# Kernel tuning notes

Hardware: AMD Instinct MI355X
Metric: run time of the kernel (lower is better)

## Reference

```python
import jax, jax.numpy as jnp
import jax.scipy.linalg as jsp
import numpy as np

# Problem dimensions (match init_kwargs P_shape/A_shape)
N = 256   # variables
M = 512   # constraints
B = 64    # batch

# OSQP ADMM hyper-parameters (fixed-rho variant of the OSQP algorithm)
SIGMA = 1e-6
RHO = 0.1
ALPHA = 1.6
N_ITERS = 500


def setup_inputs() -> dict:
    key = jax.random.key(0)
    kP, kq, kA, kc = jax.random.split(key, 4)
    # P is diagonal with strictly positive entries -> PSD (values are the nnz of P)
    P_val = jax.random.uniform(kP, (B, N), dtype=jnp.float32) + 0.1
    q_val = jax.random.normal(kq, (B, N), dtype=jnp.float32)
    # A is a dense pattern; values stored row-major as its nnz vector
    A_val = jax.random.normal(kA, (B, M * N), dtype=jnp.float32) / np.sqrt(N)
    # Feasible box: l <= u by construction
    center = jax.random.normal(kc, (B, M), dtype=jnp.float32)
    l_val = center - 1.0
    u_val = center + 1.0
    return {"P_val": P_val, "q_val": q_val, "A_val": A_val, "l_val": l_val, "u_val": u_val}


def _admm_qp(P_val, q_val, A_val, l_val, u_val):
    """Batched OSQP-style ADMM solve of min 1/2 x'Px + q'x  s.t. l <= Ax <= u.

    P is diagonal (nnz pattern = diag), A is dense (nnz pattern = full m x n).
    """
    A = A_val.reshape(B, M, N)                      # [B,m,n]
    # KKT-like matrix M_k = P + sigma*I + rho*A'A   [B,n,n]
    eye = jnp.eye(N, dtype=P_val.dtype)
    P_diag = P_val + SIGMA                          # diagonal of P + sigma*I
    Mk = RHO * jnp.einsum('bmi,bmj->bij', A, A) + jax.vmap(jnp.diag)(P_diag)
    L = jnp.linalg.cholesky(Mk)                     # [B,n,n], factor once, reuse
    Lt = jnp.swapaxes(L, -1, -2)

    def kkt_solve(rhs):                             # rhs [B,n]
        y1 = jsp.solve_triangular(L, rhs[..., None], lower=True)
        y2 = jsp.solve_triangular(Lt, y1, lower=False)
        return y2[..., 0]

    x0 = jnp.zeros((B, N), dtype=P_val.dtype)
    z0 = jnp.zeros((B, M), dtype=P_val.dtype)
    y0 = jnp.zeros((B, M), dtype=P_val.dtype)

    def step(state, _):
        x, z, y = state
        rhs = SIGMA * x - q_val + jnp.einsum('bmn,bm->bn', A, RHO * z - y)
        x_t = kkt_solve(rhs)                        # x-tilde
        z_t = jnp.einsum('bmn,bn->bm', A, x_t)      # z-tilde = A x_t
        x_new = ALPHA * x_t + (1.0 - ALPHA) * x
        z_hat = ALPHA * z_t + (1.0 - ALPHA) * z
        z_new = jnp.clip(z_hat + y / RHO, l_val, u_val)
        y_new = y + RHO * (z_hat - z_new)
        return (x_new, z_new, y_new), None

    (x, _, _), _ = jax.lax.scan(step, (x0, z0, y0), None, length=N_ITERS)
    return x


def reference(P_val, q_val, A_val, l_val, u_val):
    return _admm_qp(P_val, q_val, A_val, l_val, u_val)   # [B, n] primal solutions
```

## Files before the change

kernel.cpp:

```cpp
#include <hip/hip_runtime.h>
#include <hip/hip_fp16.h>

#define N_VAR 256
#define M_CON 512
#define BATCH 64
#define SIGMA_C 1e-6f
#define RHO_C 0.1f
#define ALPHA_C 1.6f
#define NITERS 500

__global__ __launch_bounds__(256) void k_transpose(const float* __restrict__ A,
                                                   float* __restrict__ At) {
  __shared__ float tile[32][33];
  int b = blockIdx.z;
  int n0 = blockIdx.x * 32;
  int m0 = blockIdx.y * 32;
  const float* Ab = A + (size_t)b * (M_CON * N_VAR);
  float* Atb = At + (size_t)b * (M_CON * N_VAR);
  int tx = threadIdx.x, ty = threadIdx.y;
#pragma unroll
  for (int j = 0; j < 32; j += 8)
    tile[ty + j][tx] = Ab[(size_t)(m0 + ty + j) * N_VAR + n0 + tx];
  __syncthreads();
#pragma unroll
  for (int j = 0; j < 32; j += 8)
    Atb[(size_t)(n0 + ty + j) * M_CON + m0 + tx] = tile[tx][ty + j];
}

__global__ __launch_bounds__(256) void k_ntgemm(
    const float* __restrict__ X, const float* __restrict__ Y,
    float* __restrict__ C, int J, int K,
    long long bsX, long long bsY, long long bsC, float alpha,
    const float* __restrict__ diagv, int tilesJ, int symN) {
  int b = blockIdx.y;
  int ti, tj;
  if (symN > 0) {
    int r = blockIdx.x;
    ti = 0;
    while (r >= symN - ti) { r -= (symN - ti); ++ti; }
    tj = ti + r;
  } else {
    ti = blockIdx.x / tilesJ;
    tj = blockIdx.x % tilesJ;
  }
  int i0 = ti * 128, j0 = tj * 128;
  const float* Xb = X + (size_t)b * bsX;
  const float* Yb = Y + (size_t)b * bsY;
  float* Cb = C + (size_t)b * bsC;
  __shared__ float Xs[2][16][132];
  __shared__ float Ys[2][16][132];
  int tid = threadIdx.x;
  int tx = tid & 15, ty = tid >> 4;
  int row0 = tid >> 2, k40 = (tid & 3) * 4;

  float acc[8][8];
#pragma unroll
  for (int r = 0; r < 8; ++r)
#pragma unroll
    for (int c = 0; c < 8; ++c) acc[r][c] = 0.0f;

  float4 rx0, rx1, ry0, ry1;
  auto prefetch = [&](int kk) {
    rx0 = *(const float4*)(Xb + (size_t)(i0 + row0) * K + kk + k40);
    rx1 = *(const float4*)(Xb + (size_t)(i0 + row0 + 64) * K + kk + k40);
    ry0 = *(const float4*)(Yb + (size_t)(j0 + row0) * K + kk + k40);
    ry1 = *(const float4*)(Yb + (size_t)(j0 + row0 + 64) * K + kk + k40);
  };
  auto commit = [&](int buf) {
    Xs[buf][k40 + 0][row0] = rx0.x; Xs[buf][k40 + 1][row0] = rx0.y;
    Xs[buf][k40 + 2][row0] = rx0.z; Xs[buf][k40 + 3][row0] = rx0.w;
    Xs[buf][k40 + 0][row0 + 64] = rx1.x; Xs[buf][k40 + 1][row0 + 64] = rx1.y;
    Xs[buf][k40 + 2][row0 + 64] = rx1.z; Xs[buf][k40 + 3][row0 + 64] = rx1.w;
    Ys[buf][k40 + 0][row0] = ry0.x; Ys[buf][k40 + 1][row0] = ry0.y;
    Ys[buf][k40 + 2][row0] = ry0.z; Ys[buf][k40 + 3][row0] = ry0.w;
    Ys[buf][k40 + 0][row0 + 64] = ry1.x; Ys[buf][k40 + 1][row0 + 64] = ry1.y;
    Ys[buf][k40 + 2][row0 + 64] = ry1.z; Ys[buf][k40 + 3][row0 + 64] = ry1.w;
  };

  int nkt = K >> 4;
  prefetch(0);
  commit(0);
  __syncthreads();

  for (int kt = 0; kt < nkt; ++kt) {
    int cur = kt & 1;
    if (kt + 1 < nkt) prefetch((kt + 1) * 16);
#pragma unroll
    for (int k = 0; k < 16; ++k) {
      float xr[8], yr[8];
      *(float4*)&xr[0] = *(float4*)&Xs[cur][k][ty * 8];
      *(float4*)&xr[4] = *(float4*)&Xs[cur][k][ty * 8 + 4];
      *(float4*)&yr[0] = *(float4*)&Ys[cur][k][tx * 8];
      *(float4*)&yr[4] = *(float4*)&Ys[cur][k][tx * 8 + 4];
#pragma unroll
      for (int r = 0; r < 8; ++r)
#pragma unroll
        for (int c = 0; c < 8; ++c) acc[r][c] += xr[r] * yr[c];
    }
    if (kt + 1 < nkt) commit(cur ^ 1);
    __syncthreads();
  }

#pragma unroll
  for (int r = 0; r < 8; ++r) {
    int gi = i0 + ty * 8 + r;
#pragma unroll
    for (int c = 0; c < 8; ++c) {
      int gj = j0 + tx * 8 + c;
      float val = acc[r][c] * alpha;
      if (diagv != nullptr && gi == gj) val += diagv[(size_t)b * N_VAR + gi] + SIGMA_C;
      Cb[(size_t)gi * J + gj] = val;
    }
  }
}

__global__ __launch_bounds__(256) void k_mirror(float* __restrict__ C, int n,
                                                long long bsC) {
  __shared__ float tile[32][33];
  int b = blockIdx.y;
  int idx = blockIdx.x;
  int bi = 1;
  while (idx >= bi) { idx -= bi; ++bi; }
  int bj = idx;
  float* Cb = C + (size_t)b * bsC;
  int tx = threadIdx.x & 31, ty = threadIdx.x >> 5;
#pragma unroll
  for (int j = 0; j < 32; j += 8)
    tile[ty + j][tx] = Cb[(size_t)(bj * 32 + ty + j) * n + bi * 32 + tx];
  __syncthreads();
#pragma unroll
  for (int j = 0; j < 32; j += 8)
    Cb[(size_t)(bi * 32 + ty + j) * n + bj * 32 + tx] = tile[tx][ty + j];
}

__global__ __launch_bounds__(512, 2) void k_invert(const float* __restrict__ Mk,
                                                   float* __restrict__ Mi) {
  int b = blockIdx.x;
  const float* src = Mk + (size_t)b * 65536;
  float* dst = Mi + (size_t)b * 65536;
  int t = threadIdx.x;
  int c = t & 255, rh = t >> 8;

  float a[128];
#pragma unroll
  for (int j = 0; j < 128; ++j) a[j] = src[(size_t)(rh * 128 + j) * 256 + c];

  __shared__ float colPan[256][8];
  __shared__ float rowPan[2][8][260];
  __shared__ float PiSh[64];
  __shared__ float Rp[8][260];

  int rh_s = __builtin_amdgcn_readfirstlane(rh);
  int cw_s = __builtin_amdgcn_readfirstlane((t >> 6) & 3);

  if (rh == 0) {
#pragma unroll
    for (int j = 0; j < 8; ++j) rowPan[0][j][c] = a[j];
  }
  __syncthreads();

  for (int s = 0; s < 32; ++s) {
    int kb = s * 8;
    int cur = s & 1, nxt = cur ^ 1;
    int kh = kb >> 7, kj = kb & 127;
    int khn = (kb + 8) >> 7, kjn = (kb + 8) & 127;
    bool mycol = (c >= kb) && (c < kb + 8);

    if (cw_s == (kb >> 6)) {
      if (mycol) {
        int f = c - kb;
#pragma unroll
        for (int j = 0; j < 128; ++j) colPan[rh * 128 + j][f] = a[j];
      }
    }
    if (t < 64) {
      int e = t >> 3, f = t & 7;
      float p = rowPan[cur][e][kb + f];
#pragma unroll
      for (int k2 = 0; k2 < 8; ++k2) {
        float piv = __shfl(p, k2 * 8 + k2);
        float rv = __shfl(p, k2 * 8 + f);
        float cv = __shfl(p, e * 8 + k2);
        float pivinv = 1.0f / piv;
        float srv = rv * pivinv;
        float gen = p - cv * srv;
        p = gen;
        if (e == k2) p = srv;
        if (f == k2) p = -cv * pivinv;
        if (e == k2 && f == k2) p = pivinv;
      }
      PiSh[t] = p;
    }
    __syncthreads();

    float rpan[8];
#pragma unroll
    for (int f2 = 0; f2 < 8; ++f2) rpan[f2] = rowPan[cur][f2][c];
    float rp[8];
#pragma unroll
    for (int e = 0; e < 8; ++e) {
      float4 p0 = *(const float4*)&PiSh[e * 8];
      float4 p1 = *(const float4*)&PiSh[e * 8 + 4];
      rp[e] = p0.x * rpan[0] + p0.y * rpan[1] + p0.z * rpan[2] + p0.w * rpan[3] +
              p1.x * rpan[4] + p1.y * rpan[5] + p1.z * rpan[6] + p1.w * rpan[7];
    }
    if (cw_s == (kb >> 6)) {
      if (mycol) {
        int f = c - kb;
#pragma unroll
        for (int e = 0; e < 8; ++e) rp[e] = PiSh[e * 8 + f];
      }
    }
#pragma unroll
    for (int e = 0; e < 8; ++e) Rp[e][c] = rp[e];

    bool myhalfk = (rh_s == kh);
    bool stashw = (s != 31) && (rh_s == khn);
#pragma unroll
    for (int j = 0; j < 128; ++j) {
      float4 c0 = *(const float4*)&colPan[rh * 128 + j][0];
      float4 c1 = *(const float4*)&colPan[rh * 128 + j][4];
      float aold = a[j];
      float nv = aold -
                 (c0.x * rp[0] + c0.y * rp[1] + c0.z * rp[2] + c0.w * rp[3] +
                  c1.x * rp[4] + c1.y * rp[5] + c1.z * rp[6] + c1.w * rp[7]);
      if (mycol) nv -= aold;
      if (myhalfk && j >= kj && j < kj + 8)
        nv = Rp[j - kj][c];
      a[j] = nv;
      if (stashw && j >= kjn && j < kjn + 8)
        rowPan[nxt][j - kjn][c] = nv;
    }
    __syncthreads();
  }

#pragma unroll
  for (int j = 0; j < 128; ++j) dst[(size_t)(rh * 128 + j) * 256 + c] = a[j];
}

__global__ __launch_bounds__(256) void k_matvec_h(const float* __restrict__ Mi,
                                                  const float* __restrict__ q,
                                                  float* __restrict__ h) {
  int b = blockIdx.x, t = threadIdx.x;
  __shared__ float qs[256];
  qs[t] = q[(size_t)b * 256 + t];
  __syncthreads();
  const float* Mb = Mi + (size_t)b * 65536;
  float acc = 0.0f;
  for (int k = 0; k < 256; ++k) acc += Mb[(size_t)k * 256 + t] * qs[k];
  h[(size_t)b * 256 + t] = acc;
}

__global__ __launch_bounds__(512) void k_matvec_d(const float* __restrict__ At,
                                                  const float* __restrict__ h,
                                                  float* __restrict__ d) {
  int b = blockIdx.x, t = threadIdx.x;
  __shared__ float hs[256];
  if (t < 256) hs[t] = h[(size_t)b * 256 + t];
  __syncthreads();
  const float* Ab = At + (size_t)b * 131072;
  float acc = 0.0f;
  for (int n = 0; n < 256; ++n) acc += Ab[(size_t)n * 512 + t] * hs[n];
  d[(size_t)b * 512 + t] = acc;
}

__global__ __launch_bounds__(512, 2) void k_admm4(
    const float* __restrict__ G, const float* __restrict__ dvec,
    const float* __restrict__ lv, const float* __restrict__ uv,
    unsigned long long* __restrict__ wtag, float* __restrict__ Sbuf) {
  int g = blockIdx.x;
  int b = (g & 7) + 8 * ((g >> 3) & 7);
  int s = g >> 6;
  int t = threadIdx.x;
  int r = t & 31, ck = t >> 5;
  int c0 = ck * 32;

  __shared__ __align__(16) float wloc[512];
  __shared__ float part[16][132];

  const float* Gb = G + (size_t)b * 262144;
  float Greg[4][32];
#pragma unroll
  for (int k = 0; k < 4; ++k) {
    const float* gp = Gb + (size_t)(s * 128 + r + 32 * k) * 512 + c0;
#pragma unroll
    for (int j = 0; j < 8; ++j) {
      float4 v = *(const float4*)(gp + 4 * j);
      Greg[k][4 * j + 0] = v.x; Greg[k][4 * j + 1] = v.y;
      Greg[k][4 * j + 2] = v.z; Greg[k][4 * j + 3] = v.w;
    }
  }

  float zreg = 0.0f, yreg = 0.0f, Sreg = 0.0f;
  float lreg = 0.0f, ureg = 0.0f, dreg = 0.0f;
  if (t < 128) {
    lreg = lv[(size_t)b * 512 + s * 128 + t];
    ureg = uv[(size_t)b * 512 + s * 128 + t];
    dreg = dvec[(size_t)b * 512 + s * 128 + t];
  }
  wloc[t] = 0.0f;

  unsigned long long* wt0 = wtag + (size_t)b * 512;
  unsigned long long* wt1 = wtag + 32768 + (size_t)b * 512;
  int gr = (s * 128 + t) & 511;
  const float4* wq4 = (const float4*)(wloc + c0);

  for (int it = 0; it < NITERS; ++it) {
    __syncthreads();

    float a0 = 0.f, a1 = 0.f, a2 = 0.f, a3 = 0.f;
#pragma unroll
    for (int j = 0; j < 8; ++j) {
      float4 w4 = wq4[j];
      a0 += Greg[0][4 * j + 0] * w4.x + Greg[0][4 * j + 1] * w4.y +
            Greg[0][4 * j + 2] * w4.z + Greg[0][4 * j + 3] * w4.w;
      a1 += Greg[1][4 * j + 0] * w4.x + Greg[1][4 * j + 1] * w4.y +
            Greg[1][4 * j + 2] * w4.z + Greg[1][4 * j + 3] * w4.w;
      a2 += Greg[2][4 * j + 0] * w4.x + Greg[2][4 * j + 1] * w4.y +
            Greg[2][4 * j + 2] * w4.z + Greg[2][4 * j + 3] * w4.w;
      a3 += Greg[3][4 * j + 0] * w4.x + Greg[3][4 * j + 1] * w4.y +
            Greg[3][4 * j + 2] * w4.z + Greg[3][4 * j + 3] * w4.w;
    }
    part[ck][r] = a0;
    part[ck][r + 32] = a1;
    part[ck][r + 64] = a2;
    part[ck][r + 96] = a3;
    __syncthreads();

    if (t < 128) {
      float w_old = RHO_C * zreg - yreg;
      Sreg = w_old - 0.6f * Sreg;
      float p = 0.0f;
#pragma unroll
      for (int c = 0; c < 16; ++c) p += part[c][t];
      float zt = p - dreg;
      float zh = ALPHA_C * zt + (1.0f - ALPHA_C) * zreg;
      float zc = zh + yreg * (1.0f / RHO_C);
      zc = fminf(fmaxf(zc, lreg), ureg);
      yreg += RHO_C * (zh - zc);
      zreg = zc;
      float wn = RHO_C * zreg - yreg;
      wloc[s * 128 + t] = wn;
      if (it < NITERS - 1) {
        unsigned long long pk =
            ((unsigned long long)(unsigned)(it + 1) << 32) |
            (unsigned long long)__float_as_uint(wn);
        unsigned long long* wp = ((it + 1) & 1) ? wt1 : wt0;
        __hip_atomic_store(&wp[s * 128 + t], pk, __ATOMIC_RELAXED,
                           __HIP_MEMORY_SCOPE_AGENT);
      }
    } else if (it < NITERS - 1) {
      unsigned long long* wp = ((it + 1) & 1) ? wt1 : wt0;
      unsigned want = (unsigned)(it + 1);
      unsigned long long v;
      for (;;) {
        v = __hip_atomic_load(&wp[gr], __ATOMIC_RELAXED,
                              __HIP_MEMORY_SCOPE_AGENT);
        if ((unsigned)(v >> 32) == want) break;
        __builtin_amdgcn_s_sleep(1);
      }
      wloc[gr] = __uint_as_float((unsigned)(v & 0xffffffffu));
    }
  }

  if (t < 128) Sbuf[(size_t)b * 512 + s * 128 + t] = Sreg;
}

__global__ __launch_bounds__(256) void k_final(
    const float* __restrict__ A, const float* __restrict__ q,
    const float* __restrict__ Mi, const float* __restrict__ Sbuf,
    float* __restrict__ xout) {
  int b = blockIdx.x, t = threadIdx.x;
  __shared__ float Ssh[512];
  __shared__ float uu[256];
  for (int i = t; i < 512; i += 256) Ssh[i] = Sbuf[(size_t)b * 512 + i];
  __syncthreads();
  const float* Ab = A + (size_t)b * 131072;
  float acc = 0.0f;
  for (int m = 0; m < 512; ++m) acc += Ab[(size_t)m * 256 + t] * Ssh[m];
  uu[t] = ALPHA_C * acc - q[(size_t)b * 256 + t];
  __syncthreads();
  const float* Mb = Mi + (size_t)b * 65536;
  float x = 0.0f;
  for (int kk = 0; kk < 256; ++kk) x += Mb[(size_t)kk * 256 + t] * uu[kk];
  xout[(size_t)b * 256 + t] = x;
}

extern "C" void kernel_launch(void* const* d_in, const int* in_sizes, int n_in,
                              void* d_out, int out_size, void* d_ws, size_t ws_size,
                              hipStream_t stream) {
  (void)in_sizes; (void)n_in; (void)out_size; (void)ws_size;
  const float* P = (const float*)d_in[0];
  const float* q = (const float*)d_in[1];
  const float* Av = (const float*)d_in[2];
  const float* lv = (const float*)d_in[3];
  const float* uv = (const float*)d_in[4];
  float* xout = (float*)d_out;

  float* ws = (float*)d_ws;
  float* At = ws;
  float* F  = ws;
  float* Mi = ws + 8388608;
  float* Mk = ws + 12582912;
  float* G  = ws + 12582912;
  float* hv = ws + 29360128;
  float* dv = ws + 29376512;
  float* Sbuf = ws + 29409280;
  unsigned long long* wtag = (unsigned long long*)ws;

  k_transpose<<<dim3(8, 16, 64), dim3(32, 8), 0, stream>>>(Av, At);
  k_ntgemm<<<dim3(3, 64), 256, 0, stream>>>(At, At, Mk, 256, 512,
                                            131072LL, 131072LL, 65536LL,
                                            RHO_C, P, 0, 2);
  k_mirror<<<dim3(28, 64), 256, 0, stream>>>(Mk, 256, 65536LL);
  k_invert<<<64, 512, 0, stream>>>(Mk, Mi);
  k_matvec_h<<<64, 256, 0, stream>>>(Mi, q, hv);
  k_matvec_d<<<64, 512, 0, stream>>>(At, hv, dv);
  k_ntgemm<<<dim3(8, 64), 256, 0, stream>>>(Av, Mi, F, 256, 256,
                                            131072LL, 65536LL, 131072LL,
                                            1.0f, nullptr, 2, 0);
  k_ntgemm<<<dim3(10, 64), 256, 0, stream>>>(F, Av, G, 512, 256,
                                             131072LL, 131072LL, 262144LL,
                                             1.0f, nullptr, 0, 4);
  k_mirror<<<dim3(120, 64), 256, 0, stream>>>(G, 512, 262144LL);
  k_admm4<<<256, 512, 0, stream>>>(G, dv, lv, uv, wtag, Sbuf);
  k_final<<<64, 256, 0, stream>>>(Av, q, Mi, Sbuf, xout);
}
```

Before: 1.723 ms.

## Exit ADMM loop early once z and y reach a bitwise fixed point

Each ADMM block now checks, through a ballot and a flag bit packed into the exchanged tag words, whether its z and y values and all remote w values stayed bitwise unchanged. Once the state is stationary it applies the remaining S recurrence in closed form and leaves the loop, skipping the rest of the iterations. The two small matvec kernels are also fused into one launch. Results should match exactly when the fixed point holds, but the gain depends on the inputs converging exactly, and the extra shared flags and ballot add per-iteration overhead.

```diff
diff --git a/kernel.cpp b/kernel.cpp
--- a/kernel.cpp
+++ b/kernel.cpp
@@ -238,25 +238,20 @@
   for (int j = 0; j < 128; ++j) dst[(size_t)(rh * 128 + j) * 256 + c] = a[j];
 }
 
-__global__ __launch_bounds__(256) void k_matvec_h(const float* __restrict__ Mi,
-                                                  const float* __restrict__ q,
-                                                  float* __restrict__ h) {
+__global__ __launch_bounds__(512) void k_matvec_hd(
+    const float* __restrict__ Mi, const float* __restrict__ q,
+    const float* __restrict__ At, float* __restrict__ d) {
   int b = blockIdx.x, t = threadIdx.x;
   __shared__ float qs[256];
-  qs[t] = q[(size_t)b * 256 + t];
-  __syncthreads();
-  const float* Mb = Mi + (size_t)b * 65536;
-  float acc = 0.0f;
-  for (int k = 0; k < 256; ++k) acc += Mb[(size_t)k * 256 + t] * qs[k];
-  h[(size_t)b * 256 + t] = acc;
-}
-
-__global__ __launch_bounds__(512) void k_matvec_d(const float* __restrict__ At,
-                                                  const float* __restrict__ h,
-                                                  float* __restrict__ d) {
-  int b = blockIdx.x, t = threadIdx.x;
   __shared__ float hs[256];
-  if (t < 256) hs[t] = h[(size_t)b * 256 + t];
+  if (t < 256) qs[t] = q[(size_t)b * 256 + t];
+  __syncthreads();
+  if (t < 256) {
+    const float* Mb = Mi + (size_t)b * 65536;
+    float acc = 0.0f;
+    for (int k = 0; k < 256; ++k) acc += Mb[(size_t)k * 256 + t] * qs[k];
+    hs[t] = acc;
+  }
   __syncthreads();
   const float* Ab = At + (size_t)b * 131072;
   float acc = 0.0f;
@@ -277,6 +272,8 @@
 
   __shared__ __align__(16) float wloc[512];
   __shared__ float part[16][132];
+  __shared__ int ownW[2][2];
+  __shared__ int remOK[2];
 
   const float* Gb = G + (size_t)b * 262144;
   float Greg[4][32];
@@ -299,6 +296,10 @@
     dreg = dvec[(size_t)b * 512 + s * 128 + t];
   }
   wloc[t] = 0.0f;
+  if (t == 0) {
+    ownW[0][0] = 0; ownW[0][1] = 0; ownW[1][0] = 0; ownW[1][1] = 0;
+    remOK[0] = 1; remOK[1] = 1;
+  }
 
   unsigned long long* wt0 = wtag + (size_t)b * 512;
   unsigned long long* wt1 = wtag + 32768 + (size_t)b * 512;
@@ -307,6 +308,18 @@
 
   for (int it = 0; it < NITERS; ++it) {
     __syncthreads();
+
+    {
+      int slot = it & 1;
+      if (ownW[slot][0] && ownW[slot][1] && remOK[slot]) {
+        if (t < 128) {
+          float ww = RHO_C * zreg - yreg;
+          int R = NITERS - it;
+          for (int i2 = 0; i2 < R; ++i2) Sreg = ww - 0.6f * Sreg;
+        }
+        break;
+      }
+    }
 
     float a0 = 0.f, a1 = 0.f, a2 = 0.f, a3 = 0.f;
 #pragma unroll
@@ -328,6 +341,7 @@
     __syncthreads();
 
     if (t < 128) {
+      float zold = zreg, yold = yreg;
       float w_old = RHO_C * zreg - yreg;
       Sreg = w_old - 0.6f * Sreg;
       float p = 0.0f;
@@ -339,10 +353,16 @@
       zc = fminf(fmaxf(zc, lreg), ureg);
       yreg += RHO_C * (zh - zc);
       zreg = zc;
+      bool rowst = (__float_as_uint(zreg) == __float_as_uint(zold)) &&
+                   (__float_as_uint(yreg) == __float_as_uint(yold));
+      unsigned long long bal = __ballot(rowst);
+      if ((t & 63) == 0) ownW[(it + 1) & 1][t >> 6] = (bal == ~0ull);
+      if (t == 0) remOK[it & 1] = 1;
       float wn = RHO_C * zreg - yreg;
       wloc[s * 128 + t] = wn;
       if (it < NITERS - 1) {
         unsigned long long pk =
+            ((unsigned long long)(rowst ? 1u : 0u) << 63) |
             ((unsigned long long)(unsigned)(it + 1) << 32) |
             (unsigned long long)__float_as_uint(wn);
         unsigned long long* wp = ((it + 1) & 1) ? wt1 : wt0;
@@ -356,10 +376,11 @@
       for (;;) {
         v = __hip_atomic_load(&wp[gr], __ATOMIC_RELAXED,
                               __HIP_MEMORY_SCOPE_AGENT);
-        if ((unsigned)(v >> 32) == want) break;
+        if ((unsigned)((v >> 32) & 0x7fffffffu) == want) break;
         __builtin_amdgcn_s_sleep(1);
       }
       wloc[gr] = __uint_as_float((unsigned)(v & 0xffffffffu));
+      if (!(v >> 63)) remOK[(it + 1) & 1] = 0;
     }
   }
 
@@ -403,7 +424,6 @@
   float* Mi = ws + 8388608;
   float* Mk = ws + 12582912;
   float* G  = ws + 12582912;
-  float* hv = ws + 29360128;
   float* dv = ws + 29376512;
   float* Sbuf = ws + 29409280;
   unsigned long long* wtag = (unsigned long long*)ws;
@@ -414,8 +434,7 @@
                                             RHO_C, P, 0, 2);
   k_mirror<<<dim3(28, 64), 256, 0, stream>>>(Mk, 256, 65536LL);
   k_invert<<<64, 512, 0, stream>>>(Mk, Mi);
-  k_matvec_h<<<64, 256, 0, stream>>>(Mi, q, hv);
-  k_matvec_d<<<64, 512, 0, stream>>>(At, hv, dv);
+  k_matvec_hd<<<64, 512, 0, stream>>>(Mi, q, At, dv);
   k_ntgemm<<<dim3(8, 64), 256, 0, stream>>>(Av, Mi, F, 256, 256,
                                             131072LL, 65536LL, 131072LL,
                                             1.0f, nullptr, 2, 0);
```

Result: slower. 1.777 ms (+3.2%).

## Drop transpose and mirror kernels by fusing symmetric stores into GEMMs

Applied to the files above, without the earlier changes.

Removes the explicit A transpose by adding a dedicated A^T A GEMM that reads A row-major directly and writes both the upper tile and its mirrored transpose through a shared-memory staging buffer. The separate mirror kernels for Mk and G are likewise replaced by in-epilogue transposed writes in the symmetric GEMM. The two matvec kernels are merged into one that computes h in shared memory and then d = A h using wave-level shuffle reductions. This cuts several launches and full-matrix round trips through global memory, at the cost of extra shared memory and serialized transpose-store passes in the GEMM epilogues.

```diff
diff --git a/kernel.cpp b/kernel.cpp
--- a/kernel.cpp
+++ b/kernel.cpp
@@ -9,29 +9,114 @@
 #define ALPHA_C 1.6f
 #define NITERS 500
 
-__global__ __launch_bounds__(256) void k_transpose(const float* __restrict__ A,
-                                                   float* __restrict__ At) {
-  __shared__ float tile[32][33];
-  int b = blockIdx.z;
-  int n0 = blockIdx.x * 32;
-  int m0 = blockIdx.y * 32;
-  const float* Ab = A + (size_t)b * (M_CON * N_VAR);
-  float* Atb = At + (size_t)b * (M_CON * N_VAR);
-  int tx = threadIdx.x, ty = threadIdx.y;
-#pragma unroll
-  for (int j = 0; j < 32; j += 8)
-    tile[ty + j][tx] = Ab[(size_t)(m0 + ty + j) * N_VAR + n0 + tx];
-  __syncthreads();
-#pragma unroll
-  for (int j = 0; j < 32; j += 8)
-    Atb[(size_t)(n0 + ty + j) * M_CON + m0 + tx] = tile[tx][ty + j];
+__global__ __launch_bounds__(256) void k_mkgemm(const float* __restrict__ A,
+                                                float* __restrict__ Mk,
+                                                const float* __restrict__ P) {
+  int b = blockIdx.y;
+  int r3 = blockIdx.x;
+  int ti = (r3 == 2) ? 1 : 0, tj = (r3 == 0) ? 0 : 1;
+  int i0 = ti * 128, j0 = tj * 128;
+  bool diag = (ti == tj);
+  const float* Ab = A + (size_t)b * 131072;
+  float* Cb = Mk + (size_t)b * 65536;
+
+  __shared__ float Xs[2][16][132];
+  __shared__ float Ys[2][16][132];
+  __shared__ float TB[16][132];
+
+  int tid = threadIdx.x;
+  int tx = tid & 15, ty = tid >> 4;
+
+  float acc[8][8];
+#pragma unroll
+  for (int r = 0; r < 8; ++r)
+#pragma unroll
+    for (int c = 0; c < 8; ++c) acc[r][c] = 0.0f;
+
+  float4 px[2], py[2];
+  auto prefetch = [&](int kk) {
+#pragma unroll
+    for (int v = 0; v < 2; ++v) {
+      int idx = v * 256 + tid;
+      int mm = idx >> 5, f4 = idx & 31;
+      px[v] = *(const float4*)(Ab + (size_t)(kk + mm) * 256 + i0 + 4 * f4);
+      if (!diag)
+        py[v] = *(const float4*)(Ab + (size_t)(kk + mm) * 256 + j0 + 4 * f4);
+    }
+  };
+  auto commit = [&](int buf) {
+#pragma unroll
+    for (int v = 0; v < 2; ++v) {
+      int idx = v * 256 + tid;
+      int mm = idx >> 5, f4 = idx & 31;
+      *(float4*)&Xs[buf][mm][4 * f4] = px[v];
+      if (!diag) *(float4*)&Ys[buf][mm][4 * f4] = py[v];
+    }
+  };
+
+  prefetch(0);
+  commit(0);
+  __syncthreads();
+
+  for (int kt = 0; kt < 32; ++kt) {
+    int cur = kt & 1;
+    if (kt + 1 < 32) prefetch((kt + 1) * 16);
+#pragma unroll
+    for (int k = 0; k < 16; ++k) {
+      float xr[8], yr[8];
+      *(float4*)&xr[0] = *(float4*)&Xs[cur][k][ty * 8];
+      *(float4*)&xr[4] = *(float4*)&Xs[cur][k][ty * 8 + 4];
+      const float* yb = diag ? &Xs[cur][k][0] : &Ys[cur][k][0];
+      *(float4*)&yr[0] = *(const float4*)&yb[tx * 8];
+      *(float4*)&yr[4] = *(const float4*)&yb[tx * 8 + 4];
+#pragma unroll
+      for (int r = 0; r < 8; ++r)
+#pragma unroll
+        for (int c = 0; c < 8; ++c) acc[r][c] += xr[r] * yr[c];
+    }
+    if (kt + 1 < 32) commit(cur ^ 1);
+    __syncthreads();
+  }
+
+#pragma unroll
+  for (int r = 0; r < 8; ++r) {
+    int gi = i0 + ty * 8 + r;
+#pragma unroll
+    for (int c = 0; c < 8; ++c) {
+      int gj = j0 + tx * 8 + c;
+      float val = acc[r][c] * RHO_C;
+      if (gi == gj) val += P[(size_t)b * 256 + gi] + SIGMA_C;
+      Cb[(size_t)gi * 256 + gj] = val;
+      acc[r][c] = val;
+    }
+  }
+  if (!diag) {
+    for (int ci = 0; ci < 8; ++ci) {
+      __syncthreads();
+      if ((ty >> 1) == ci) {
+        int base = (ty & 1) * 8;
+#pragma unroll
+        for (int r = 0; r < 8; ++r)
+#pragma unroll
+          for (int c = 0; c < 8; ++c) TB[base + r][tx * 8 + c] = acc[r][c];
+      }
+      __syncthreads();
+      int jj = tid >> 1, half = tid & 1;
+      float o[8];
+#pragma unroll
+      for (int e = 0; e < 8; ++e) o[e] = TB[8 * half + e][jj];
+      float* dst = Cb + (size_t)(j0 + jj) * 256 + i0 + ci * 16 + 8 * half;
+      *(float4*)dst = make_float4(o[0], o[1], o[2], o[3]);
+      *(float4*)(dst + 4) = make_float4(o[4], o[5], o[6], o[7]);
+    }
+  }
 }
 
 __global__ __launch_bounds__(256) void k_ntgemm(
     const float* __restrict__ X, const float* __restrict__ Y,
     float* __restrict__ C, int J, int K,
     long long bsX, long long bsY, long long bsC, float alpha,
-    const float* __restrict__ diagv, int tilesJ, int symN) {
+    int tilesJ, int symN) {
   int b = blockIdx.y;
   int ti, tj;
   if (symN > 0) {
@@ -49,6 +134,7 @@
   float* Cb = C + (size_t)b * bsC;
   __shared__ float Xs[2][16][132];
   __shared__ float Ys[2][16][132];
+  __shared__ float TB[16][132];
   int tid = threadIdx.x;
   int tx = tid & 15, ty = tid >> 4;
   int row0 = tid >> 2, k40 = (tid & 3) * 4;
@@ -108,29 +194,30 @@
     for (int c = 0; c < 8; ++c) {
       int gj = j0 + tx * 8 + c;
       float val = acc[r][c] * alpha;
-      if (diagv != nullptr && gi == gj) val += diagv[(size_t)b * N_VAR + gi] + SIGMA_C;
       Cb[(size_t)gi * J + gj] = val;
-    }
-  }
-}
-
-__global__ __launch_bounds__(256) void k_mirror(float* __restrict__ C, int n,
-                                                long long bsC) {
-  __shared__ float tile[32][33];
-  int b = blockIdx.y;
-  int idx = blockIdx.x;
-  int bi = 1;
-  while (idx >= bi) { idx -= bi; ++bi; }
-  int bj = idx;
-  float* Cb = C + (size_t)b * bsC;
-  int tx = threadIdx.x & 31, ty = threadIdx.x >> 5;
-#pragma unroll
-  for (int j = 0; j < 32; j += 8)
-    tile[ty + j][tx] = Cb[(size_t)(bj * 32 + ty + j) * n + bi * 32 + tx];
-  __syncthreads();
-#pragma unroll
-  for (int j = 0; j < 32; j += 8)
-    Cb[(size_t)(bi * 32 + ty + j) * n + bj * 32 + tx] = tile[tx][ty + j];
+      acc[r][c] = val;
+    }
+  }
+  if (symN > 0 && ti != tj) {
+    for (int ci = 0; ci < 8; ++ci) {
+      __syncthreads();
+      if ((ty >> 1) == ci) {
+        int base = (ty & 1) * 8;
+#pragma unroll
+        for (int r = 0; r < 8; ++r)
+#pragma unroll
+          for (int c = 0; c < 8; ++c) TB[base + r][tx * 8 + c] = acc[r][c];
+      }
+      __syncthreads();
+      int jj = tid >> 1, half = tid & 1;
+      float o[8];
+#pragma unroll
+      for (int e = 0; e < 8; ++e) o[e] = TB[8 * half + e][jj];
+      float* dst = Cb + (size_t)(j0 + jj) * J + i0 + ci * 16 + 8 * half;
+      *(float4*)dst = make_float4(o[0], o[1], o[2], o[3]);
+      *(float4*)(dst + 4) = make_float4(o[4], o[5], o[6], o[7]);
+    }
+  }
 }
 
 __global__ __launch_bounds__(512, 2) void k_invert(const float* __restrict__ Mk,
@@ -238,30 +325,32 @@
   for (int j = 0; j < 128; ++j) dst[(size_t)(rh * 128 + j) * 256 + c] = a[j];
 }
 
-__global__ __launch_bounds__(256) void k_matvec_h(const float* __restrict__ Mi,
-                                                  const float* __restrict__ q,
-                                                  float* __restrict__ h) {
+__global__ __launch_bounds__(512) void k_matvec_hd(
+    const float* __restrict__ Mi, const float* __restrict__ q,
+    const float* __restrict__ A, float* __restrict__ d) {
   int b = blockIdx.x, t = threadIdx.x;
   __shared__ float qs[256];
-  qs[t] = q[(size_t)b * 256 + t];
-  __syncthreads();
-  const float* Mb = Mi + (size_t)b * 65536;
-  float acc = 0.0f;
-  for (int k = 0; k < 256; ++k) acc += Mb[(size_t)k * 256 + t] * qs[k];
-  h[(size_t)b * 256 + t] = acc;
-}
-
-__global__ __launch_bounds__(512) void k_matvec_d(const float* __restrict__ At,
-                                                  const float* __restrict__ h,
-                                                  float* __restrict__ d) {
-  int b = blockIdx.x, t = threadIdx.x;
-  __shared__ float hs[256];
-  if (t < 256) hs[t] = h[(size_t)b * 256 + t];
-  __syncthreads();
-  const float* Ab = At + (size_t)b * 131072;
-  float acc = 0.0f;
-  for (int n = 0; n < 256; ++n) acc += Ab[(size_t)n * 512 + t] * hs[n];
-  d[(size_t)b * 512 + t] = acc;
+  __shared__ __align__(16) float hs[256];
+  if (t < 256) qs[t] = q[(size_t)b * 256 + t];
+  __syncthreads();
+  if (t < 256) {
+    const float* Mb = Mi + (size_t)b * 65536;
+    float acc = 0.0f;
+    for (int k = 0; k < 256; ++k) acc += Mb[(size_t)k * 256 + t] * qs[k];
+    hs[t] = acc;
+  }
+  __syncthreads();
+  int wv = t >> 6, l = t & 63;
+  const float* Ab = A + (size_t)b * 131072;
+  float4 h4 = *(const float4*)&hs[4 * l];
+  for (int i = 0; i < 64; ++i) {
+    int m = wv * 64 + i;
+    float4 a4 = *(const float4*)(Ab + (size_t)m * 256 + 4 * l);
+    float p = a4.x * h4.x + a4.y * h4.y + a4.z * h4.z + a4.w * h4.w;
+#pragma unroll
+    for (int off = 32; off >= 1; off >>= 1) p += __shfl_down(p, off);
+    if (l == 0) d[(size_t)b * 512 + m] = p;
+  }
 }
 
 __global__ __launch_bounds__(512, 2) void k_admm4(
@@ -398,31 +487,23 @@
   float* xout = (float*)d_out;
 
   float* ws = (float*)d_ws;
-  float* At = ws;
   float* F  = ws;
   float* Mi = ws + 8388608;
   float* Mk = ws + 12582912;
   float* G  = ws + 12582912;
-  float* hv = ws + 29360128;
   float* dv = ws + 29376512;
   float* Sbuf = ws + 29409280;
   unsigned long long* wtag = (unsigned long long*)ws;
 
-  k_transpose<<<dim3(8, 16, 64), dim3(32, 8), 0, stream>>>(Av, At);
-  k_ntgemm<<<dim3(3, 64), 256, 0, stream>>>(At, At, Mk, 256, 512,
-                                            131072LL, 131072LL, 65536LL,
-                                            RHO_C, P, 0, 2);
-  k_mirror<<<dim3(28, 64), 256, 0, stream>>>(Mk, 256, 65536LL);
+  k_mkgemm<<<dim3(3, 64), 256, 0, stream>>>(Av, Mk, P);
   k_invert<<<64, 512, 0, stream>>>(Mk, Mi);
-  k_matvec_h<<<64, 256, 0, stream>>>(Mi, q, hv);
-  k_matvec_d<<<64, 512, 0, stream>>>(At, hv, dv);
+  k_matvec_hd<<<64, 512, 0, stream>>>(Mi, q, Av, dv);
   k_ntgemm<<<dim3(8, 64), 256, 0, stream>>>(Av, Mi, F, 256, 256,
                                             131072LL, 65536LL, 131072LL,
-                                            1.0f, nullptr, 2, 0);
+                                            1.0f, 2, 0);
   k_ntgemm<<<dim3(10, 64), 256, 0, stream>>>(F, Av, G, 512, 256,
                                              131072LL, 131072LL, 262144LL,
-                                             1.0f, nullptr, 0, 4);
-  k_mirror<<<dim3(120, 64), 256, 0, stream>>>(G, 512, 262144LL);
+                                             1.0f, 0, 4);
   k_admm4<<<256, 512, 0, stream>>>(G, dv, lv, uv, wtag, Sbuf);
   k_final<<<64, 256, 0, stream>>>(Av, q, Mi, Sbuf, xout);
 }
```

After: 1.712 ms. About the same (-0.6%).
